# Kernel tuning notes

Hardware: AMD Instinct MI355X
Metric: run time of the kernel (lower is better)

Reference implementation:

```python
import jax, jax.numpy as jnp
import numpy as np

B, D_IN, D_Z, D_H, D_T, D_REC = 8192, 1024, 256, 256, 16, 256


def _softplus_beta(x, beta):
    # torch F.softplus(x, beta) = (1/beta) * log(1 + exp(beta*x))
    return jax.nn.softplus(beta * x) / beta


def setup_inputs() -> dict:
    key = jax.random.key(0)
    ks = jax.random.split(key, 17)
    w = lambda k, o, i: jax.random.normal(k, (o, i), jnp.float32) * (1.0 / np.sqrt(i))
    return {
        "I_t": jax.random.uniform(ks[0], (B, D_IN), jnp.float32),
        "h_m_1": jax.random.uniform(ks[1], (B, D_H), jnp.float32),
        "z_m_1": jax.random.uniform(ks[2], (B, D_Z), jnp.float32),
        "theta_m_1": jax.random.normal(ks[3], (B, D_T), jnp.float32),
        "eps_z": jax.random.normal(ks[4], (B, D_Z), jnp.float32),
        "eps_zhat": jax.random.normal(ks[5], (B, D_Z), jnp.float32),
        "W_post_mu": w(ks[6], D_Z, D_IN),
        "W_post_lv": w(ks[7], D_Z, D_IN),
        "W_z2h": w(ks[8], D_H, D_Z),
        "W_h2h": w(ks[9], D_H, D_H),
        "W_prior_mu": w(ks[10], D_Z, D_H),
        "W_prior_lv": w(ks[11], D_Z, D_H),
        "W_i2t": w(ks[12], D_T, D_IN),
        "W_vip2t": w(ks[13], D_T, D_Z),
        "W_t2z": w(ks[14], D_Z, D_T),
        "W_rec1": w(ks[15], D_REC, D_Z),
        "W_rec2": w(ks[16], D_IN, D_REC),
    }


def reference(I_t, h_m_1, z_m_1, theta_m_1, eps_z, eps_zhat,
              W_post_mu, W_post_lv, W_z2h, W_h2h, W_prior_mu, W_prior_lv,
              W_i2t, W_vip2t, W_t2z, W_rec1, W_rec2):
    relu = jax.nn.relu
    # prior pathway (perception_only=True branch)
    mu_p = relu(h_m_1 @ W_prior_mu.T)                       # [B, D_Z]
    sigma_p = _softplus_beta(h_m_1 @ W_prior_lv.T, 1.2)     # [B, D_Z]
    # theta dynamics; vip_to_theta has Positive parametrization -> relu(W)
    theta_h = (0.5 * theta_m_1 + 0.1 * (I_t @ W_i2t.T)
               - jax.lax.stop_gradient(sigma_p) @ relu(W_vip2t).T)  # [B, D_T]
    theta = 0.001 * _softplus_beta(theta_h, 0.5)
    # posterior + reparameterized sample
    mu_q = relu(I_t @ W_post_mu.T)
    sigma_q = relu(I_t @ W_post_lv.T)
    raw_z = jnp.clip(mu_q + eps_z * sigma_q, 0.0, 1.0)
    thresholds = 10.0 * (theta @ relu(W_t2z).T)             # Positive parametrization
    z = relu(raw_z - thresholds)                            # [B, D_Z]
    # reconstruction (two bias-free linears + sigmoid)
    I_hat = jax.nn.sigmoid((z @ W_rec1.T) @ W_rec2.T)       # [B, D_IN]
    # higher-state update and prior sample
    h = relu(z_m_1 @ W_z2h.T + h_m_1 @ W_h2h.T)             # [B, D_H]
    z_hat = mu_p + eps_zhat * sigma_p                       # [B, D_Z]
    # losses (as in torch forward)
    spatial = jnp.mean((I_t - I_hat) ** 2)
    temporal = jnp.mean((jax.lax.stop_gradient(z) - z_hat) ** 2)
    energy = jnp.mean(jnp.abs(z))
    return (I_hat, z, h, z_hat, spatial, temporal, energy)
```

## Files before the change

kernel.cpp:

```cpp
#include <hip/hip_runtime.h>
#include <math.h>

#define BB 8192
#define DIN 1024
#define DZ 256
#define DH 256
#define DT 16
#define DREC 256

#define OFF_IHAT 0
#define OFF_Z    (BB * DIN)
#define OFF_H    (OFF_Z + BB * DZ)
#define OFF_ZHAT (OFF_H + BB * DH)
#define OFF_SCAL (OFF_ZHAT + BB * DZ)

typedef unsigned short u16;
typedef __attribute__((ext_vector_type(8))) unsigned short u16x8;
typedef __attribute__((ext_vector_type(8))) __bf16 bf16x8;
typedef __attribute__((ext_vector_type(4))) float f32x4;

#define WS_HBF   0
#define WS_ZM1BF 2097152
#define WS_W     4194304
#define W_PM  (WS_W + 0)
#define W_PL  (W_PM + 262144)
#define W_Z2H (W_PL + 262144)
#define W_H2H (W_Z2H + 65536)
#define W_PRM (W_H2H + 65536)
#define W_PRL (W_PRM + 65536)
#define W_I2T (W_PRL + 65536)
#define W_VIP (W_I2T + 16384)
#define W_R1  (W_VIP + 4096)
#define W_R2  (W_R1 + 65536)
#define WS_THETA_BYTES 10657792

#define LDA 72

__device__ inline u16 f2bf(float f) {
  unsigned u = __builtin_bit_cast(unsigned, f);
  u += 0x7fff + ((u >> 16) & 1);
  return (u16)(u >> 16);
}

__device__ inline float softplus_stable(float y) {
  return (y > 20.f) ? y : log1pf(expf(y));
}

__device__ inline float block_sum256(float v, float* rbuf) {
#pragma unroll
  for (int off = 32; off > 0; off >>= 1) v += __shfl_down(v, off, 64);
  __syncthreads();
  if ((threadIdx.x & 63) == 0) rbuf[threadIdx.x >> 6] = v;
  __syncthreads();
  return rbuf[0] + rbuf[1] + rbuf[2] + rbuf[3];
}

__global__ __launch_bounds__(256) void k_cvt(
    const float* __restrict__ I_t, const float* __restrict__ h_m_1,
    const float* __restrict__ z_m_1, const float* __restrict__ Wpm,
    const float* __restrict__ Wpl, const float* __restrict__ Wz2h,
    const float* __restrict__ Wh2h, const float* __restrict__ Wprm,
    const float* __restrict__ Wprl, const float* __restrict__ Wi2t,
    const float* __restrict__ Wv, const float* __restrict__ Wr1,
    const float* __restrict__ Wr2, u16* __restrict__ dstI,
    u16* __restrict__ dstW) {
  const int S1 = 8388608, S2 = 10485760, S3 = 12582912, S4 = 12845056,
            S5 = 13107200, S6 = 13172736, S7 = 13238272, S8 = 13303808,
            S9 = 13369344, S10 = 13385728, S11 = 13389824, S12 = 13455360,
            S13 = 13717504;
  int nchunk = S13 / 8;
  for (int c = blockIdx.x * 256 + threadIdx.x; c < nchunk;
       c += gridDim.x * 256) {
    int f = c * 8;
    const float* src;
    float scale = 1.f;
    bool nrelu = false;
    u16* dst;
    if (f < S1)       { src = I_t  + f;        dst = dstI + f; }
    else {
      dst = dstW + (f - S1);
      if (f < S2)       src = h_m_1 + (f - S1);
      else if (f < S3)  src = z_m_1 + (f - S2);
      else if (f < S4)  src = Wpm  + (f - S3);
      else if (f < S5)  src = Wpl  + (f - S4);
      else if (f < S6)  src = Wz2h + (f - S5);
      else if (f < S7)  src = Wh2h + (f - S6);
      else if (f < S8)  src = Wprm + (f - S7);
      else if (f < S9)  src = Wprl + (f - S8);
      else if (f < S10) { src = Wi2t + (f - S9);  scale = 0.1f; }
      else if (f < S11) { src = Wv   + (f - S10); nrelu = true; }
      else if (f < S12) src = Wr1  + (f - S11);
      else              src = Wr2  + (f - S12);
    }
    float4 v0 = *(const float4*)(src);
    float4 v1 = *(const float4*)(src + 4);
    float vals[8] = {v0.x, v0.y, v0.z, v0.w, v1.x, v1.y, v1.z, v1.w};
    u16x8 o;
#pragma unroll
    for (int j = 0; j < 8; ++j) {
      float x = vals[j];
      x = nrelu ? -fmaxf(x, 0.f) : x * scale;
      o[j] = f2bf(x);
    }
    *(u16x8*)(dst) = o;
  }
}

template <int K, bool TWO>
__device__ inline void mfma_gemm(const u16* __restrict__ A,
                                 const u16* __restrict__ B0,
                                 const u16* __restrict__ B1, int row0,
                                 int col0, f32x4 (&acc)[2][4],
                                 f32x4 (&acc2)[2][4], u16* As, u16* Bs0,
                                 u16* Bs1) {
  const int tid = threadIdx.x;
  const int lane = tid & 63;
  const int w = tid >> 6;
  const int frow = lane & 15;
  const int fq = lane >> 4;

  for (int k0 = 0; k0 < K; k0 += 64) {
    __syncthreads();
#pragma unroll
    for (int i = 0; i < 4; ++i) {
      int c = tid + 256 * i;
      int r = c >> 3, kc = c & 7;
      u16x8 v = *(const u16x8*)(A + (size_t)(row0 + r) * K + k0 + kc * 8);
      *(u16x8*)(As + r * LDA + kc * 8) = v;
    }
#pragma unroll
    for (int i = 0; i < 2; ++i) {
      int c = tid + 256 * i;
      int r = c >> 3, kc = c & 7;
      *(u16x8*)(Bs0 + r * LDA + kc * 8) =
          *(const u16x8*)(B0 + (size_t)(col0 + r) * K + k0 + kc * 8);
      if (TWO)
        *(u16x8*)(Bs1 + r * LDA + kc * 8) =
            *(const u16x8*)(B1 + (size_t)(col0 + r) * K + k0 + kc * 8);
    }
    __syncthreads();
#pragma unroll
    for (int ks = 0; ks < 2; ++ks) {
      bf16x8 af[2], bf[4], bf2[4];
#pragma unroll
      for (int mi = 0; mi < 2; ++mi)
        af[mi] = __builtin_bit_cast(
            bf16x8, *(const u16x8*)(As + (w * 32 + mi * 16 + frow) * LDA +
                                    fq * 8 + ks * 32));
#pragma unroll
      for (int ni = 0; ni < 4; ++ni) {
        bf[ni] = __builtin_bit_cast(
            bf16x8,
            *(const u16x8*)(Bs0 + (ni * 16 + frow) * LDA + fq * 8 + ks * 32));
        if (TWO)
          bf2[ni] = __builtin_bit_cast(
              bf16x8, *(const u16x8*)(Bs1 + (ni * 16 + frow) * LDA + fq * 8 +
                                      ks * 32));
      }
#pragma unroll
      for (int mi = 0; mi < 2; ++mi)
#pragma unroll
        for (int ni = 0; ni < 4; ++ni) {
          acc[mi][ni] = __builtin_amdgcn_mfma_f32_16x16x32_bf16(
              af[mi], bf[ni], acc[mi][ni], 0, 0, 0);
          if (TWO)
            acc2[mi][ni] = __builtin_amdgcn_mfma_f32_16x16x32_bf16(
                af[mi], bf2[ni], acc2[mi][ni], 0, 0, 0);
        }
    }
  }
}

#define EPILOGUE_IDX()                          \
  const int tid = threadIdx.x;                  \
  const int lane = tid & 63;                    \
  const int w = tid >> 6;                       \
  const int frow = lane & 15;                   \
  const int fq = lane >> 4;                     \
  (void)tid

__global__ __launch_bounds__(256) void k_h(const u16* __restrict__ zm1_bf,
                                           const u16* __restrict__ h_bf,
                                           const u16* __restrict__ Wz2h,
                                           const u16* __restrict__ Wh2h,
                                           float* __restrict__ h_out) {
  __shared__ __align__(16) u16 As[128 * LDA];
  __shared__ __align__(16) u16 Bs0[64 * LDA];
  int col0 = blockIdx.x * 64, row0 = blockIdx.y * 128;
  f32x4 acc[2][4];
#pragma unroll
  for (int mi = 0; mi < 2; ++mi)
#pragma unroll
    for (int ni = 0; ni < 4; ++ni) acc[mi][ni] = (f32x4){0.f, 0.f, 0.f, 0.f};
  mfma_gemm<DZ, false>(zm1_bf, Wz2h, nullptr, row0, col0, acc, acc, As, Bs0, Bs0);
  mfma_gemm<DH, false>(h_bf, Wh2h, nullptr, row0, col0, acc, acc, As, Bs0, Bs0);
  EPILOGUE_IDX();
#pragma unroll
  for (int mi = 0; mi < 2; ++mi)
#pragma unroll
    for (int ni = 0; ni < 4; ++ni)
#pragma unroll
      for (int r = 0; r < 4; ++r) {
        int m = row0 + w * 32 + mi * 16 + fq * 4 + r;
        int n = col0 + ni * 16 + frow;
        h_out[(size_t)m * DH + n] = fmaxf(acc[mi][ni][r], 0.f);
      }
}

__global__ __launch_bounds__(256) void k_prior(
    const u16* __restrict__ h_bf, const u16* __restrict__ Wpm,
    const u16* __restrict__ Wpl, const float* __restrict__ eps_zhat,
    float* __restrict__ zhat_out, u16* __restrict__ sigma_bf) {
  __shared__ __align__(16) u16 As[128 * LDA];
  __shared__ __align__(16) u16 Bs0[64 * LDA];
  __shared__ __align__(16) u16 Bs1[64 * LDA];
  int col0 = blockIdx.x * 64, row0 = blockIdx.y * 128;
  f32x4 acc[2][4], acc2[2][4];
#pragma unroll
  for (int mi = 0; mi < 2; ++mi)
#pragma unroll
    for (int ni = 0; ni < 4; ++ni) {
      acc[mi][ni] = (f32x4){0.f, 0.f, 0.f, 0.f};
      acc2[mi][ni] = (f32x4){0.f, 0.f, 0.f, 0.f};
    }
  mfma_gemm<DH, true>(h_bf, Wpm, Wpl, row0, col0, acc, acc2, As, Bs0, Bs1);
  EPILOGUE_IDX();
#pragma unroll
  for (int mi = 0; mi < 2; ++mi)
#pragma unroll
    for (int ni = 0; ni < 4; ++ni)
#pragma unroll
      for (int r = 0; r < 4; ++r) {
        int m = row0 + w * 32 + mi * 16 + fq * 4 + r;
        int n = col0 + ni * 16 + frow;
        float mu = fmaxf(acc[mi][ni][r], 0.f);
        float sig = softplus_stable(1.2f * acc2[mi][ni][r]) * (1.f / 1.2f);
        zhat_out[(size_t)m * DZ + n] =
            mu + eps_zhat[(size_t)m * DZ + n] * sig;
        sigma_bf[(size_t)m * DZ + n] = f2bf(sig);
      }
}

__global__ __launch_bounds__(256) void k_theta(
    const u16* __restrict__ I_bf, const u16* __restrict__ Wi2t,
    const u16* __restrict__ sigma_bf, const u16* __restrict__ Wv,
    const float* __restrict__ theta_m_1, float* __restrict__ theta_ws) {
  const int tid = threadIdx.x;
  const int lane = tid & 63;
  const int w = tid >> 6;
  const int frow = lane & 15;
  const int fq = lane >> 4;
  const int m0 = blockIdx.x * 64 + w * 16;
  f32x4 acc = (f32x4){0.f, 0.f, 0.f, 0.f};
  const u16* arow = I_bf + (size_t)(m0 + frow) * DIN + fq * 8;
  const u16* brow = Wi2t + (size_t)frow * DIN + fq * 8;
#pragma unroll
  for (int ks = 0; ks < DIN / 32; ++ks) {
    bf16x8 a = __builtin_bit_cast(bf16x8, *(const u16x8*)(arow + ks * 32));
    bf16x8 b = __builtin_bit_cast(bf16x8, *(const u16x8*)(brow + ks * 32));
    acc = __builtin_amdgcn_mfma_f32_16x16x32_bf16(a, b, acc, 0, 0, 0);
  }
  const u16* arow2 = sigma_bf + (size_t)(m0 + frow) * DZ + fq * 8;
  const u16* brow2 = Wv + (size_t)frow * DZ + fq * 8;
#pragma unroll
  for (int ks = 0; ks < DZ / 32; ++ks) {
    bf16x8 a = __builtin_bit_cast(bf16x8, *(const u16x8*)(arow2 + ks * 32));
    bf16x8 b = __builtin_bit_cast(bf16x8, *(const u16x8*)(brow2 + ks * 32));
    acc = __builtin_amdgcn_mfma_f32_16x16x32_bf16(a, b, acc, 0, 0, 0);
  }
#pragma unroll
  for (int r = 0; r < 4; ++r) {
    int m = m0 + fq * 4 + r;
    float th = 0.5f * theta_m_1[(size_t)m * DT + frow] + acc[r];
    theta_ws[(size_t)m * DT + frow] = 0.002f * softplus_stable(0.5f * th);
  }
}

__global__ __launch_bounds__(256) void k_post(
    const u16* __restrict__ I_bf, const u16* __restrict__ Wpm,
    const u16* __restrict__ Wpl, const float* __restrict__ eps_z,
    const float* __restrict__ theta_ws, const float* __restrict__ W_t2z,
    const float* __restrict__ zhat, float* __restrict__ z_out,
    u16* __restrict__ z_bf, float* __restrict__ scal) {
  __shared__ __align__(16) u16 As[128 * LDA];
  __shared__ __align__(16) u16 Bs0[64 * LDA];
  __shared__ __align__(16) u16 Bs1[64 * LDA];
  __shared__ float rbuf[4];
  int col0 = blockIdx.x * 64, row0 = blockIdx.y * 128;
  f32x4 acc[2][4], acc2[2][4];
#pragma unroll
  for (int mi = 0; mi < 2; ++mi)
#pragma unroll
    for (int ni = 0; ni < 4; ++ni) {
      acc[mi][ni] = (f32x4){0.f, 0.f, 0.f, 0.f};
      acc2[mi][ni] = (f32x4){0.f, 0.f, 0.f, 0.f};
    }
  mfma_gemm<DIN, true>(I_bf, Wpm, Wpl, row0, col0, acc, acc2, As, Bs0, Bs1);
  EPILOGUE_IDX();
  __syncthreads();
  float* th_s = (float*)As;
  float* wt_s = (float*)Bs0;
  for (int idx = tid; idx < 128 * 16; idx += 256) {
    int r = idx >> 4, j = idx & 15;
    th_s[r * 17 + j] = theta_ws[(size_t)(row0 + r) * DT + j];
  }
  for (int idx = tid; idx < 64 * 16; idx += 256) {
    int n = idx >> 4, j = idx & 15;
    wt_s[n * 17 + j] = 10.f * fmaxf(W_t2z[(col0 + n) * DT + j], 0.f);
  }
  __syncthreads();
  float tsum = 0.f, esum = 0.f;
#pragma unroll
  for (int mi = 0; mi < 2; ++mi)
#pragma unroll
    for (int ni = 0; ni < 4; ++ni)
#pragma unroll
      for (int r = 0; r < 4; ++r) {
        int lr = w * 32 + mi * 16 + fq * 4 + r;
        int ln = ni * 16 + frow;
        int m = row0 + lr;
        int n = col0 + ln;
        float mu = fmaxf(acc[mi][ni][r], 0.f);
        float sq = fmaxf(acc2[mi][ni][r], 0.f);
        float raw = mu + eps_z[(size_t)m * DZ + n] * sq;
        raw = fminf(fmaxf(raw, 0.f), 1.f);
        float thr = 0.f;
#pragma unroll
        for (int j = 0; j < 16; ++j)
          thr = fmaf(th_s[lr * 17 + j], wt_s[ln * 17 + j], thr);
        float zz = fmaxf(raw - thr, 0.f);
        z_out[(size_t)m * DZ + n] = zz;
        z_bf[(size_t)m * DZ + n] = f2bf(zz);
        float d = zz - zhat[(size_t)m * DZ + n];
        tsum += d * d;
        esum += zz;
      }
  float t = block_sum256(tsum, rbuf);
  if (tid == 0) atomicAdd(scal + 1, t * (1.f / ((float)BB * DZ)));
  float e = block_sum256(esum, rbuf);
  if (tid == 0) atomicAdd(scal + 2, e * (1.f / ((float)BB * DZ)));
}

__global__ __launch_bounds__(256) void k_rec1(const u16* __restrict__ z_bf,
                                              const u16* __restrict__ Wr1,
                                              u16* __restrict__ r1_bf) {
  __shared__ __align__(16) u16 As[128 * LDA];
  __shared__ __align__(16) u16 Bs0[64 * LDA];
  int col0 = blockIdx.x * 64, row0 = blockIdx.y * 128;
  f32x4 acc[2][4];
#pragma unroll
  for (int mi = 0; mi < 2; ++mi)
#pragma unroll
    for (int ni = 0; ni < 4; ++ni) acc[mi][ni] = (f32x4){0.f, 0.f, 0.f, 0.f};
  mfma_gemm<DZ, false>(z_bf, Wr1, nullptr, row0, col0, acc, acc, As, Bs0, Bs0);
  EPILOGUE_IDX();
#pragma unroll
  for (int mi = 0; mi < 2; ++mi)
#pragma unroll
    for (int ni = 0; ni < 4; ++ni)
#pragma unroll
      for (int r = 0; r < 4; ++r) {
        int m = row0 + w * 32 + mi * 16 + fq * 4 + r;
        int n = col0 + ni * 16 + frow;
        r1_bf[(size_t)m * DREC + n] = f2bf(acc[mi][ni][r]);
      }
}

__global__ __launch_bounds__(256) void k_rec2(const u16* __restrict__ r1_bf,
                                              const u16* __restrict__ Wr2,
                                              const float* __restrict__ I_t,
                                              float* __restrict__ ihat_out,
                                              float* __restrict__ scal) {
  __shared__ __align__(16) u16 As[128 * LDA];
  __shared__ __align__(16) u16 Bs0[64 * LDA];
  __shared__ float rbuf[4];
  int col0 = blockIdx.x * 64, row0 = blockIdx.y * 128;
  f32x4 acc[2][4];
#pragma unroll
  for (int mi = 0; mi < 2; ++mi)
#pragma unroll
    for (int ni = 0; ni < 4; ++ni) acc[mi][ni] = (f32x4){0.f, 0.f, 0.f, 0.f};
  mfma_gemm<DREC, false>(r1_bf, Wr2, nullptr, row0, col0, acc, acc, As, Bs0, Bs0);
  EPILOGUE_IDX();
  float lsum = 0.f;
#pragma unroll
  for (int mi = 0; mi < 2; ++mi)
#pragma unroll
    for (int ni = 0; ni < 4; ++ni)
#pragma unroll
      for (int r = 0; r < 4; ++r) {
        int m = row0 + w * 32 + mi * 16 + fq * 4 + r;
        int n = col0 + ni * 16 + frow;
        float ih = 1.f / (1.f + expf(-acc[mi][ni][r]));
        ihat_out[(size_t)m * DIN + n] = ih;
        float d = I_t[(size_t)m * DIN + n] - ih;
        lsum += d * d;
      }
  float s = block_sum256(lsum, rbuf);
  if (tid == 0) atomicAdd(scal + 0, s * (1.f / ((float)BB * DIN)));
}

extern "C" void kernel_launch(void* const* d_in, const int* in_sizes, int n_in,
                              void* d_out, int out_size, void* d_ws,
                              size_t ws_size, hipStream_t stream) {
  const float* I_t       = (const float*)d_in[0];
  const float* h_m_1     = (const float*)d_in[1];
  const float* z_m_1     = (const float*)d_in[2];
  const float* theta_m_1 = (const float*)d_in[3];
  const float* eps_z     = (const float*)d_in[4];
  const float* eps_zhat  = (const float*)d_in[5];
  const float* W_post_mu = (const float*)d_in[6];
  const float* W_post_lv = (const float*)d_in[7];
  const float* W_z2h     = (const float*)d_in[8];
  const float* W_h2h     = (const float*)d_in[9];
  const float* W_prior_mu= (const float*)d_in[10];
  const float* W_prior_lv= (const float*)d_in[11];
  const float* W_i2t     = (const float*)d_in[12];
  const float* W_vip2t   = (const float*)d_in[13];
  const float* W_t2z     = (const float*)d_in[14];
  const float* W_rec1    = (const float*)d_in[15];
  const float* W_rec2    = (const float*)d_in[16];

  float* out = (float*)d_out;
  float* ihat = out + OFF_IHAT;
  float* zout = out + OFF_Z;
  float* hout = out + OFF_H;
  float* zhat = out + OFF_ZHAT;
  float* scal = out + OFF_SCAL;

  u16* ws_u = (u16*)d_ws;
  u16* I_bf = (u16*)ihat;
  u16* h_bf = ws_u + WS_HBF;
  u16* zm1_bf = ws_u + WS_ZM1BF;
  u16* sigma_bf = zm1_bf;
  u16* r1_bf = zm1_bf;
  u16* z_bf = h_bf;
  float* theta_ws = (float*)((char*)d_ws + WS_THETA_BYTES);

  hipMemsetAsync(scal, 0, 3 * sizeof(float), stream);

  k_cvt<<<2048, 256, 0, stream>>>(I_t, h_m_1, z_m_1, W_post_mu, W_post_lv,
                                  W_z2h, W_h2h, W_prior_mu, W_prior_lv, W_i2t,
                                  W_vip2t, W_rec1, W_rec2, I_bf,
                                  ws_u + WS_HBF);

  dim3 g256(DZ / 64, BB / 128);
  dim3 g1024(DIN / 64, BB / 128);

  k_h<<<g256, 256, 0, stream>>>(zm1_bf, h_bf, ws_u + W_Z2H, ws_u + W_H2H, hout);
  k_prior<<<g256, 256, 0, stream>>>(h_bf, ws_u + W_PRM, ws_u + W_PRL, eps_zhat,
                                    zhat, sigma_bf);
  k_theta<<<BB / 64, 256, 0, stream>>>(I_bf, ws_u + W_I2T, sigma_bf,
                                       ws_u + W_VIP, theta_m_1, theta_ws);
  k_post<<<g256, 256, 0, stream>>>(I_bf, ws_u + W_PM, ws_u + W_PL, eps_z,
                                   theta_ws, W_t2z, zhat, zout, z_bf, scal);
  k_rec1<<<g256, 256, 0, stream>>>(z_bf, ws_u + W_R1, r1_bf);
  k_rec2<<<g1024, 256, 0, stream>>>(r1_bf, ws_u + W_R2, I_t, ihat, scal);
}
```

Measured before the change: 285.1 us.

## Fuse fp32-to-bf16 conversion into GEMM staging and merge kernels

Removes the separate conversion kernel and instead converts fp32 inputs and weights to bf16 while staging tiles into LDS inside each GEMM. The h, prior and theta computations are fused: k_hp computes h and the prior from a shared h_m_1 tile, and k_post computes theta in-kernel alongside the posterior GEMM, cutting the launch count from seven to four. Tiles shrink from 128 to 64 rows, which doubles the grid size. The cost is that I_t and the weights are now read as fp32 and reconverted by every block that uses them, and each staged fp32 load is wider.

```diff
diff --git a/kernel.cpp b/kernel.cpp
--- a/kernel.cpp
+++ b/kernel.cpp
@@ -14,27 +14,16 @@
 #define OFF_ZHAT (OFF_H + BB * DH)
 #define OFF_SCAL (OFF_ZHAT + BB * DZ)
 
+#define WS_SIGMA 0
+#define WS_ZBF   2097152
+#define WS_R1    4194304
+
+#define LDA 72
+
 typedef unsigned short u16;
 typedef __attribute__((ext_vector_type(8))) unsigned short u16x8;
 typedef __attribute__((ext_vector_type(8))) __bf16 bf16x8;
 typedef __attribute__((ext_vector_type(4))) float f32x4;
-
-#define WS_HBF   0
-#define WS_ZM1BF 2097152
-#define WS_W     4194304
-#define W_PM  (WS_W + 0)
-#define W_PL  (W_PM + 262144)
-#define W_Z2H (W_PL + 262144)
-#define W_H2H (W_Z2H + 65536)
-#define W_PRM (W_H2H + 65536)
-#define W_PRL (W_PRM + 65536)
-#define W_I2T (W_PRL + 65536)
-#define W_VIP (W_I2T + 16384)
-#define W_R1  (W_VIP + 4096)
-#define W_R2  (W_R1 + 65536)
-#define WS_THETA_BYTES 10657792
-
-#define LDA 72
 
 __device__ inline u16 f2bf(float f) {
   unsigned u = __builtin_bit_cast(unsigned, f);
@@ -55,45 +44,44 @@
   return rbuf[0] + rbuf[1] + rbuf[2] + rbuf[3];
 }
 
-__global__ __launch_bounds__(256) void k_cvt(
-    const float* __restrict__ I_t, const float* __restrict__ h_m_1,
-    const float* __restrict__ z_m_1, const float* __restrict__ Wpm,
-    const float* __restrict__ Wpl, const float* __restrict__ Wz2h,
-    const float* __restrict__ Wh2h, const float* __restrict__ Wprm,
-    const float* __restrict__ Wprl, const float* __restrict__ Wi2t,
-    const float* __restrict__ Wv, const float* __restrict__ Wr1,
-    const float* __restrict__ Wr2, u16* __restrict__ dstI,
-    u16* __restrict__ dstW) {
-  const int S1 = 8388608, S2 = 10485760, S3 = 12582912, S4 = 12845056,
-            S5 = 13107200, S6 = 13172736, S7 = 13238272, S8 = 13303808,
-            S9 = 13369344, S10 = 13385728, S11 = 13389824, S12 = 13455360,
-            S13 = 13717504;
-  int nchunk = S13 / 8;
-  for (int c = blockIdx.x * 256 + threadIdx.x; c < nchunk;
-       c += gridDim.x * 256) {
-    int f = c * 8;
-    const float* src;
-    float scale = 1.f;
-    bool nrelu = false;
-    u16* dst;
-    if (f < S1)       { src = I_t  + f;        dst = dstI + f; }
-    else {
-      dst = dstW + (f - S1);
-      if (f < S2)       src = h_m_1 + (f - S1);
-      else if (f < S3)  src = z_m_1 + (f - S2);
-      else if (f < S4)  src = Wpm  + (f - S3);
-      else if (f < S5)  src = Wpl  + (f - S4);
-      else if (f < S6)  src = Wz2h + (f - S5);
-      else if (f < S7)  src = Wh2h + (f - S6);
-      else if (f < S8)  src = Wprm + (f - S7);
-      else if (f < S9)  src = Wprl + (f - S8);
-      else if (f < S10) { src = Wi2t + (f - S9);  scale = 0.1f; }
-      else if (f < S11) { src = Wv   + (f - S10); nrelu = true; }
-      else if (f < S12) src = Wr1  + (f - S11);
-      else              src = Wr2  + (f - S12);
-    }
-    float4 v0 = *(const float4*)(src);
-    float4 v1 = *(const float4*)(src + 4);
+__device__ inline void stage64(u16* lds, const float* __restrict__ src,
+                               int row0, int ld, int k0, float scale) {
+  const int tid = threadIdx.x;
+#pragma unroll
+  for (int i = 0; i < 2; ++i) {
+    int idx = tid + 256 * i;
+    int r = idx >> 3, kc = idx & 7;
+    const float* p = src + (size_t)(row0 + r) * ld + k0 + kc * 8;
+    float4 v0 = *(const float4*)p;
+    float4 v1 = *(const float4*)(p + 4);
+    float vals[8] = {v0.x, v0.y, v0.z, v0.w, v1.x, v1.y, v1.z, v1.w};
+    u16x8 o;
+#pragma unroll
+    for (int j = 0; j < 8; ++j) o[j] = f2bf(vals[j] * scale);
+    *(u16x8*)(lds + r * LDA + kc * 8) = o;
+  }
+}
+
+__device__ inline void stage64_bf(u16* lds, const u16* __restrict__ src,
+                                  int row0, int ld, int k0) {
+  const int tid = threadIdx.x;
+#pragma unroll
+  for (int i = 0; i < 2; ++i) {
+    int idx = tid + 256 * i;
+    int r = idx >> 3, kc = idx & 7;
+    *(u16x8*)(lds + r * LDA + kc * 8) =
+        *(const u16x8*)(src + (size_t)(row0 + r) * ld + k0 + kc * 8);
+  }
+}
+
+__device__ inline void stage16(u16* lds, const float* __restrict__ src, int ld,
+                               int k0, float scale, bool nrelu) {
+  const int tid = threadIdx.x;
+  if (tid < 128) {
+    int r = tid >> 3, kc = tid & 7;
+    const float* p = src + (size_t)r * ld + k0 + kc * 8;
+    float4 v0 = *(const float4*)p;
+    float4 v1 = *(const float4*)(p + 4);
     float vals[8] = {v0.x, v0.y, v0.z, v0.w, v1.x, v1.y, v1.z, v1.w};
     u16x8 o;
 #pragma unroll
@@ -102,207 +90,141 @@
       x = nrelu ? -fmaxf(x, 0.f) : x * scale;
       o[j] = f2bf(x);
     }
-    *(u16x8*)(dst) = o;
-  }
-}
-
-template <int K, bool TWO>
-__device__ inline void mfma_gemm(const u16* __restrict__ A,
-                                 const u16* __restrict__ B0,
-                                 const u16* __restrict__ B1, int row0,
-                                 int col0, f32x4 (&acc)[2][4],
-                                 f32x4 (&acc2)[2][4], u16* As, u16* Bs0,
-                                 u16* Bs1) {
-  const int tid = threadIdx.x;
-  const int lane = tid & 63;
-  const int w = tid >> 6;
-  const int frow = lane & 15;
-  const int fq = lane >> 4;
-
-  for (int k0 = 0; k0 < K; k0 += 64) {
-    __syncthreads();
-#pragma unroll
-    for (int i = 0; i < 4; ++i) {
-      int c = tid + 256 * i;
-      int r = c >> 3, kc = c & 7;
-      u16x8 v = *(const u16x8*)(A + (size_t)(row0 + r) * K + k0 + kc * 8);
-      *(u16x8*)(As + r * LDA + kc * 8) = v;
-    }
-#pragma unroll
-    for (int i = 0; i < 2; ++i) {
-      int c = tid + 256 * i;
-      int r = c >> 3, kc = c & 7;
-      *(u16x8*)(Bs0 + r * LDA + kc * 8) =
-          *(const u16x8*)(B0 + (size_t)(col0 + r) * K + k0 + kc * 8);
-      if (TWO)
-        *(u16x8*)(Bs1 + r * LDA + kc * 8) =
-            *(const u16x8*)(B1 + (size_t)(col0 + r) * K + k0 + kc * 8);
-    }
-    __syncthreads();
-#pragma unroll
-    for (int ks = 0; ks < 2; ++ks) {
-      bf16x8 af[2], bf[4], bf2[4];
-#pragma unroll
-      for (int mi = 0; mi < 2; ++mi)
-        af[mi] = __builtin_bit_cast(
-            bf16x8, *(const u16x8*)(As + (w * 32 + mi * 16 + frow) * LDA +
-                                    fq * 8 + ks * 32));
+    *(u16x8*)(lds + r * LDA + kc * 8) = o;
+  }
+}
+
+__device__ inline bf16x8 frag(const u16* lds, int row, int off) {
+  return __builtin_bit_cast(bf16x8, *(const u16x8*)(lds + row * LDA + off));
+}
+
+#define MFMA __builtin_amdgcn_mfma_f32_16x16x32_bf16
+
+__global__ __launch_bounds__(256) void k_hp(
+    const float* __restrict__ h_m_1, const float* __restrict__ z_m_1,
+    const float* __restrict__ Wh2h, const float* __restrict__ Wprm,
+    const float* __restrict__ Wprl, const float* __restrict__ Wz2h,
+    const float* __restrict__ eps_zhat, float* __restrict__ h_out,
+    float* __restrict__ zhat_out, u16* __restrict__ sigma_bf) {
+  __shared__ __align__(16) u16 As[64 * LDA], B0s[64 * LDA], B1s[64 * LDA],
+      B2s[64 * LDA];
+  const int col0 = blockIdx.x * 64, row0 = blockIdx.y * 64;
+  const int tid = threadIdx.x, lane = tid & 63, w = tid >> 6;
+  const int frow = lane & 15, fq = lane >> 4;
+  f32x4 acch[4], accm[4], accs[4];
+#pragma unroll
+  for (int ni = 0; ni < 4; ++ni) {
+    acch[ni] = (f32x4){0.f, 0.f, 0.f, 0.f};
+    accm[ni] = (f32x4){0.f, 0.f, 0.f, 0.f};
+    accs[ni] = (f32x4){0.f, 0.f, 0.f, 0.f};
+  }
+  for (int k0 = 0; k0 < DH; k0 += 64) {
+    __syncthreads();
+    stage64(As, h_m_1, row0, DH, k0, 1.f);
+    stage64(B0s, Wh2h, col0, DH, k0, 1.f);
+    stage64(B1s, Wprm, col0, DH, k0, 1.f);
+    stage64(B2s, Wprl, col0, DH, k0, 1.f);
+    __syncthreads();
+#pragma unroll
+    for (int ks = 0; ks < 2; ++ks) {
+      int off = ks * 32 + fq * 8;
+      bf16x8 a = frag(As, w * 16 + frow, off);
 #pragma unroll
       for (int ni = 0; ni < 4; ++ni) {
-        bf[ni] = __builtin_bit_cast(
-            bf16x8,
-            *(const u16x8*)(Bs0 + (ni * 16 + frow) * LDA + fq * 8 + ks * 32));
-        if (TWO)
-          bf2[ni] = __builtin_bit_cast(
-              bf16x8, *(const u16x8*)(Bs1 + (ni * 16 + frow) * LDA + fq * 8 +
-                                      ks * 32));
+        acch[ni] = MFMA(a, frag(B0s, ni * 16 + frow, off), acch[ni], 0, 0, 0);
+        accm[ni] = MFMA(a, frag(B1s, ni * 16 + frow, off), accm[ni], 0, 0, 0);
+        accs[ni] = MFMA(a, frag(B2s, ni * 16 + frow, off), accs[ni], 0, 0, 0);
       }
-#pragma unroll
-      for (int mi = 0; mi < 2; ++mi)
-#pragma unroll
-        for (int ni = 0; ni < 4; ++ni) {
-          acc[mi][ni] = __builtin_amdgcn_mfma_f32_16x16x32_bf16(
-              af[mi], bf[ni], acc[mi][ni], 0, 0, 0);
-          if (TWO)
-            acc2[mi][ni] = __builtin_amdgcn_mfma_f32_16x16x32_bf16(
-                af[mi], bf2[ni], acc2[mi][ni], 0, 0, 0);
-        }
-    }
-  }
-}
-
-#define EPILOGUE_IDX()                          \
-  const int tid = threadIdx.x;                  \
-  const int lane = tid & 63;                    \
-  const int w = tid >> 6;                       \
-  const int frow = lane & 15;                   \
-  const int fq = lane >> 4;                     \
-  (void)tid
-
-__global__ __launch_bounds__(256) void k_h(const u16* __restrict__ zm1_bf,
-                                           const u16* __restrict__ h_bf,
-                                           const u16* __restrict__ Wz2h,
-                                           const u16* __restrict__ Wh2h,
-                                           float* __restrict__ h_out) {
-  __shared__ __align__(16) u16 As[128 * LDA];
-  __shared__ __align__(16) u16 Bs0[64 * LDA];
-  int col0 = blockIdx.x * 64, row0 = blockIdx.y * 128;
-  f32x4 acc[2][4];
-#pragma unroll
-  for (int mi = 0; mi < 2; ++mi)
-#pragma unroll
-    for (int ni = 0; ni < 4; ++ni) acc[mi][ni] = (f32x4){0.f, 0.f, 0.f, 0.f};
-  mfma_gemm<DZ, false>(zm1_bf, Wz2h, nullptr, row0, col0, acc, acc, As, Bs0, Bs0);
-  mfma_gemm<DH, false>(h_bf, Wh2h, nullptr, row0, col0, acc, acc, As, Bs0, Bs0);
-  EPILOGUE_IDX();
-#pragma unroll
-  for (int mi = 0; mi < 2; ++mi)
-#pragma unroll
-    for (int ni = 0; ni < 4; ++ni)
-#pragma unroll
-      for (int r = 0; r < 4; ++r) {
-        int m = row0 + w * 32 + mi * 16 + fq * 4 + r;
-        int n = col0 + ni * 16 + frow;
-        h_out[(size_t)m * DH + n] = fmaxf(acc[mi][ni][r], 0.f);
+    }
+  }
+  for (int k0 = 0; k0 < DZ; k0 += 64) {
+    __syncthreads();
+    stage64(As, z_m_1, row0, DZ, k0, 1.f);
+    stage64(B0s, Wz2h, col0, DZ, k0, 1.f);
+    __syncthreads();
+#pragma unroll
+    for (int ks = 0; ks < 2; ++ks) {
+      int off = ks * 32 + fq * 8;
+      bf16x8 a = frag(As, w * 16 + frow, off);
+#pragma unroll
+      for (int ni = 0; ni < 4; ++ni)
+        acch[ni] = MFMA(a, frag(B0s, ni * 16 + frow, off), acch[ni], 0, 0, 0);
+    }
+  }
+#pragma unroll
+  for (int ni = 0; ni < 4; ++ni)
+#pragma unroll
+    for (int r = 0; r < 4; ++r) {
+      int m = row0 + w * 16 + fq * 4 + r;
+      int n = col0 + ni * 16 + frow;
+      h_out[(size_t)m * DH + n] = fmaxf(acch[ni][r], 0.f);
+      float sig = softplus_stable(1.2f * accs[ni][r]) * (1.f / 1.2f);
+      float mu = fmaxf(accm[ni][r], 0.f);
+      zhat_out[(size_t)m * DZ + n] = mu + eps_zhat[(size_t)m * DZ + n] * sig;
+      sigma_bf[(size_t)m * DZ + n] = f2bf(sig);
+    }
+}
+
+__global__ __launch_bounds__(256) void k_post(
+    const float* __restrict__ I_t, const float* __restrict__ Wpm,
+    const float* __restrict__ Wpl, const float* __restrict__ Wi2t,
+    const float* __restrict__ Wv, const u16* __restrict__ sigma_bf,
+    const float* __restrict__ theta_m_1, const float* __restrict__ W_t2z,
+    const float* __restrict__ eps_z, const float* __restrict__ zhat,
+    float* __restrict__ z_out, u16* __restrict__ z_bf,
+    float* __restrict__ scal) {
+  __shared__ __align__(16) u16 As[64 * LDA], B0s[64 * LDA], B1s[64 * LDA],
+      Bts[16 * LDA];
+  __shared__ float rbuf[4];
+  const int col0 = blockIdx.x * 64, row0 = blockIdx.y * 64;
+  const int tid = threadIdx.x, lane = tid & 63, w = tid >> 6;
+  const int frow = lane & 15, fq = lane >> 4;
+  f32x4 accm[4], accs[4];
+  f32x4 acct = (f32x4){0.f, 0.f, 0.f, 0.f};
+#pragma unroll
+  for (int ni = 0; ni < 4; ++ni) {
+    accm[ni] = (f32x4){0.f, 0.f, 0.f, 0.f};
+    accs[ni] = (f32x4){0.f, 0.f, 0.f, 0.f};
+  }
+  for (int k0 = 0; k0 < DIN; k0 += 64) {
+    __syncthreads();
+    stage64(As, I_t, row0, DIN, k0, 1.f);
+    stage64(B0s, Wpm, col0, DIN, k0, 1.f);
+    stage64(B1s, Wpl, col0, DIN, k0, 1.f);
+    stage16(Bts, Wi2t, DIN, k0, 0.1f, false);
+    __syncthreads();
+#pragma unroll
+    for (int ks = 0; ks < 2; ++ks) {
+      int off = ks * 32 + fq * 8;
+      bf16x8 a = frag(As, w * 16 + frow, off);
+#pragma unroll
+      for (int ni = 0; ni < 4; ++ni) {
+        accm[ni] = MFMA(a, frag(B0s, ni * 16 + frow, off), accm[ni], 0, 0, 0);
+        accs[ni] = MFMA(a, frag(B1s, ni * 16 + frow, off), accs[ni], 0, 0, 0);
       }
-}
-
-__global__ __launch_bounds__(256) void k_prior(
-    const u16* __restrict__ h_bf, const u16* __restrict__ Wpm,
-    const u16* __restrict__ Wpl, const float* __restrict__ eps_zhat,
-    float* __restrict__ zhat_out, u16* __restrict__ sigma_bf) {
-  __shared__ __align__(16) u16 As[128 * LDA];
-  __shared__ __align__(16) u16 Bs0[64 * LDA];
-  __shared__ __align__(16) u16 Bs1[64 * LDA];
-  int col0 = blockIdx.x * 64, row0 = blockIdx.y * 128;
-  f32x4 acc[2][4], acc2[2][4];
-#pragma unroll
-  for (int mi = 0; mi < 2; ++mi)
-#pragma unroll
-    for (int ni = 0; ni < 4; ++ni) {
-      acc[mi][ni] = (f32x4){0.f, 0.f, 0.f, 0.f};
-      acc2[mi][ni] = (f32x4){0.f, 0.f, 0.f, 0.f};
-    }
-  mfma_gemm<DH, true>(h_bf, Wpm, Wpl, row0, col0, acc, acc2, As, Bs0, Bs1);
-  EPILOGUE_IDX();
-#pragma unroll
-  for (int mi = 0; mi < 2; ++mi)
-#pragma unroll
-    for (int ni = 0; ni < 4; ++ni)
-#pragma unroll
-      for (int r = 0; r < 4; ++r) {
-        int m = row0 + w * 32 + mi * 16 + fq * 4 + r;
-        int n = col0 + ni * 16 + frow;
-        float mu = fmaxf(acc[mi][ni][r], 0.f);
-        float sig = softplus_stable(1.2f * acc2[mi][ni][r]) * (1.f / 1.2f);
-        zhat_out[(size_t)m * DZ + n] =
-            mu + eps_zhat[(size_t)m * DZ + n] * sig;
-        sigma_bf[(size_t)m * DZ + n] = f2bf(sig);
-      }
-}
-
-__global__ __launch_bounds__(256) void k_theta(
-    const u16* __restrict__ I_bf, const u16* __restrict__ Wi2t,
-    const u16* __restrict__ sigma_bf, const u16* __restrict__ Wv,
-    const float* __restrict__ theta_m_1, float* __restrict__ theta_ws) {
-  const int tid = threadIdx.x;
-  const int lane = tid & 63;
-  const int w = tid >> 6;
-  const int frow = lane & 15;
-  const int fq = lane >> 4;
-  const int m0 = blockIdx.x * 64 + w * 16;
-  f32x4 acc = (f32x4){0.f, 0.f, 0.f, 0.f};
-  const u16* arow = I_bf + (size_t)(m0 + frow) * DIN + fq * 8;
-  const u16* brow = Wi2t + (size_t)frow * DIN + fq * 8;
-#pragma unroll
-  for (int ks = 0; ks < DIN / 32; ++ks) {
-    bf16x8 a = __builtin_bit_cast(bf16x8, *(const u16x8*)(arow + ks * 32));
-    bf16x8 b = __builtin_bit_cast(bf16x8, *(const u16x8*)(brow + ks * 32));
-    acc = __builtin_amdgcn_mfma_f32_16x16x32_bf16(a, b, acc, 0, 0, 0);
-  }
-  const u16* arow2 = sigma_bf + (size_t)(m0 + frow) * DZ + fq * 8;
-  const u16* brow2 = Wv + (size_t)frow * DZ + fq * 8;
-#pragma unroll
-  for (int ks = 0; ks < DZ / 32; ++ks) {
-    bf16x8 a = __builtin_bit_cast(bf16x8, *(const u16x8*)(arow2 + ks * 32));
-    bf16x8 b = __builtin_bit_cast(bf16x8, *(const u16x8*)(brow2 + ks * 32));
-    acc = __builtin_amdgcn_mfma_f32_16x16x32_bf16(a, b, acc, 0, 0, 0);
-  }
-#pragma unroll
-  for (int r = 0; r < 4; ++r) {
-    int m = m0 + fq * 4 + r;
-    float th = 0.5f * theta_m_1[(size_t)m * DT + frow] + acc[r];
-    theta_ws[(size_t)m * DT + frow] = 0.002f * softplus_stable(0.5f * th);
-  }
-}
-
-__global__ __launch_bounds__(256) void k_post(
-    const u16* __restrict__ I_bf, const u16* __restrict__ Wpm,
-    const u16* __restrict__ Wpl, const float* __restrict__ eps_z,
-    const float* __restrict__ theta_ws, const float* __restrict__ W_t2z,
-    const float* __restrict__ zhat, float* __restrict__ z_out,
-    u16* __restrict__ z_bf, float* __restrict__ scal) {
-  __shared__ __align__(16) u16 As[128 * LDA];
-  __shared__ __align__(16) u16 Bs0[64 * LDA];
-  __shared__ __align__(16) u16 Bs1[64 * LDA];
-  __shared__ float rbuf[4];
-  int col0 = blockIdx.x * 64, row0 = blockIdx.y * 128;
-  f32x4 acc[2][4], acc2[2][4];
-#pragma unroll
-  for (int mi = 0; mi < 2; ++mi)
-#pragma unroll
-    for (int ni = 0; ni < 4; ++ni) {
-      acc[mi][ni] = (f32x4){0.f, 0.f, 0.f, 0.f};
-      acc2[mi][ni] = (f32x4){0.f, 0.f, 0.f, 0.f};
-    }
-  mfma_gemm<DIN, true>(I_bf, Wpm, Wpl, row0, col0, acc, acc2, As, Bs0, Bs1);
-  EPILOGUE_IDX();
+      acct = MFMA(a, frag(Bts, frow, off), acct, 0, 0, 0);
+    }
+  }
+  for (int k0 = 0; k0 < DZ; k0 += 64) {
+    __syncthreads();
+    stage64_bf(As, sigma_bf, row0, DZ, k0);
+    stage16(Bts, Wv, DZ, k0, 1.f, true);
+    __syncthreads();
+#pragma unroll
+    for (int ks = 0; ks < 2; ++ks) {
+      int off = ks * 32 + fq * 8;
+      acct = MFMA(frag(As, w * 16 + frow, off), frag(Bts, frow, off), acct, 0,
+                  0, 0);
+    }
+  }
   __syncthreads();
   float* th_s = (float*)As;
-  float* wt_s = (float*)Bs0;
-  for (int idx = tid; idx < 128 * 16; idx += 256) {
-    int r = idx >> 4, j = idx & 15;
-    th_s[r * 17 + j] = theta_ws[(size_t)(row0 + r) * DT + j];
+  float* wt_s = (float*)B0s;
+#pragma unroll
+  for (int r = 0; r < 4; ++r) {
+    int lr = w * 16 + fq * 4 + r;
+    float th = 0.5f * theta_m_1[(size_t)(row0 + lr) * DT + frow] + acct[r];
+    th_s[lr * 17 + frow] = 0.002f * softplus_stable(0.5f * th);
   }
   for (int idx = tid; idx < 64 * 16; idx += 256) {
     int n = idx >> 4, j = idx & 15;
@@ -311,30 +233,28 @@
   __syncthreads();
   float tsum = 0.f, esum = 0.f;
 #pragma unroll
-  for (int mi = 0; mi < 2; ++mi)
-#pragma unroll
-    for (int ni = 0; ni < 4; ++ni)
-#pragma unroll
-      for (int r = 0; r < 4; ++r) {
-        int lr = w * 32 + mi * 16 + fq * 4 + r;
-        int ln = ni * 16 + frow;
-        int m = row0 + lr;
-        int n = col0 + ln;
-        float mu = fmaxf(acc[mi][ni][r], 0.f);
-        float sq = fmaxf(acc2[mi][ni][r], 0.f);
-        float raw = mu + eps_z[(size_t)m * DZ + n] * sq;
-        raw = fminf(fmaxf(raw, 0.f), 1.f);
-        float thr = 0.f;
-#pragma unroll
-        for (int j = 0; j < 16; ++j)
-          thr = fmaf(th_s[lr * 17 + j], wt_s[ln * 17 + j], thr);
-        float zz = fmaxf(raw - thr, 0.f);
-        z_out[(size_t)m * DZ + n] = zz;
-        z_bf[(size_t)m * DZ + n] = f2bf(zz);
-        float d = zz - zhat[(size_t)m * DZ + n];
-        tsum += d * d;
-        esum += zz;
-      }
+  for (int ni = 0; ni < 4; ++ni)
+#pragma unroll
+    for (int r = 0; r < 4; ++r) {
+      int lr = w * 16 + fq * 4 + r;
+      int ln = ni * 16 + frow;
+      int m = row0 + lr;
+      int n = col0 + ln;
+      float mu = fmaxf(accm[ni][r], 0.f);
+      float sq = fmaxf(accs[ni][r], 0.f);
+      float raw = mu + eps_z[(size_t)m * DZ + n] * sq;
+      raw = fminf(fmaxf(raw, 0.f), 1.f);
+      float thr = 0.f;
+#pragma unroll
+      for (int j = 0; j < 16; ++j)
+        thr = fmaf(th_s[lr * 17 + j], wt_s[ln * 17 + j], thr);
+      float zz = fmaxf(raw - thr, 0.f);
+      z_out[(size_t)m * DZ + n] = zz;
+      z_bf[(size_t)m * DZ + n] = f2bf(zz);
+      float d = zz - zhat[(size_t)m * DZ + n];
+      tsum += d * d;
+      esum += zz;
+    }
   float t = block_sum256(tsum, rbuf);
   if (tid == 0) atomicAdd(scal + 1, t * (1.f / ((float)BB * DZ)));
   float e = block_sum256(esum, rbuf);
@@ -342,60 +262,78 @@
 }
 
 __global__ __launch_bounds__(256) void k_rec1(const u16* __restrict__ z_bf,
-                                              const u16* __restrict__ Wr1,
+                                              const float* __restrict__ Wr1,
                                               u16* __restrict__ r1_bf) {
-  __shared__ __align__(16) u16 As[128 * LDA];
-  __shared__ __align__(16) u16 Bs0[64 * LDA];
-  int col0 = blockIdx.x * 64, row0 = blockIdx.y * 128;
-  f32x4 acc[2][4];
-#pragma unroll
-  for (int mi = 0; mi < 2; ++mi)
-#pragma unroll
-    for (int ni = 0; ni < 4; ++ni) acc[mi][ni] = (f32x4){0.f, 0.f, 0.f, 0.f};
-  mfma_gemm<DZ, false>(z_bf, Wr1, nullptr, row0, col0, acc, acc, As, Bs0, Bs0);
-  EPILOGUE_IDX();
-#pragma unroll
-  for (int mi = 0; mi < 2; ++mi)
-#pragma unroll
-    for (int ni = 0; ni < 4; ++ni)
-#pragma unroll
-      for (int r = 0; r < 4; ++r) {
-        int m = row0 + w * 32 + mi * 16 + fq * 4 + r;
-        int n = col0 + ni * 16 + frow;
-        r1_bf[(size_t)m * DREC + n] = f2bf(acc[mi][ni][r]);
-      }
+  __shared__ __align__(16) u16 As[64 * LDA], B0s[64 * LDA];
+  const int col0 = blockIdx.x * 64, row0 = blockIdx.y * 64;
+  const int tid = threadIdx.x, lane = tid & 63, w = tid >> 6;
+  const int frow = lane & 15, fq = lane >> 4;
+  f32x4 acc[4];
+#pragma unroll
+  for (int ni = 0; ni < 4; ++ni) acc[ni] = (f32x4){0.f, 0.f, 0.f, 0.f};
+  for (int k0 = 0; k0 < DZ; k0 += 64) {
+    __syncthreads();
+    stage64_bf(As, z_bf, row0, DZ, k0);
+    stage64(B0s, Wr1, col0, DZ, k0, 1.f);
+    __syncthreads();
+#pragma unroll
+    for (int ks = 0; ks < 2; ++ks) {
+      int off = ks * 32 + fq * 8;
+      bf16x8 a = frag(As, w * 16 + frow, off);
+#pragma unroll
+      for (int ni = 0; ni < 4; ++ni)
+        acc[ni] = MFMA(a, frag(B0s, ni * 16 + frow, off), acc[ni], 0, 0, 0);
+    }
+  }
+#pragma unroll
+  for (int ni = 0; ni < 4; ++ni)
+#pragma unroll
+    for (int r = 0; r < 4; ++r) {
+      int m = row0 + w * 16 + fq * 4 + r;
+      int n = col0 + ni * 16 + frow;
+      r1_bf[(size_t)m * DREC + n] = f2bf(acc[ni][r]);
+    }
 }
 
 __global__ __launch_bounds__(256) void k_rec2(const u16* __restrict__ r1_bf,
-                                              const u16* __restrict__ Wr2,
+                                              const float* __restrict__ Wr2,
                                               const float* __restrict__ I_t,
                                               float* __restrict__ ihat_out,
                                               float* __restrict__ scal) {
-  __shared__ __align__(16) u16 As[128 * LDA];
-  __shared__ __align__(16) u16 Bs0[64 * LDA];
+  __shared__ __align__(16) u16 As[64 * LDA], B0s[64 * LDA];
   __shared__ float rbuf[4];
-  int col0 = blockIdx.x * 64, row0 = blockIdx.y * 128;
-  f32x4 acc[2][4];
-#pragma unroll
-  for (int mi = 0; mi < 2; ++mi)
-#pragma unroll
-    for (int ni = 0; ni < 4; ++ni) acc[mi][ni] = (f32x4){0.f, 0.f, 0.f, 0.f};
-  mfma_gemm<DREC, false>(r1_bf, Wr2, nullptr, row0, col0, acc, acc, As, Bs0, Bs0);
-  EPILOGUE_IDX();
+  const int col0 = blockIdx.x * 64, row0 = blockIdx.y * 64;
+  const int tid = threadIdx.x, lane = tid & 63, w = tid >> 6;
+  const int frow = lane & 15, fq = lane >> 4;
+  f32x4 acc[4];
+#pragma unroll
+  for (int ni = 0; ni < 4; ++ni) acc[ni] = (f32x4){0.f, 0.f, 0.f, 0.f};
+  for (int k0 = 0; k0 < DREC; k0 += 64) {
+    __syncthreads();
+    stage64_bf(As, r1_bf, row0, DREC, k0);
+    stage64(B0s, Wr2, col0, DREC, k0, 1.f);
+    __syncthreads();
+#pragma unroll
+    for (int ks = 0; ks < 2; ++ks) {
+      int off = ks * 32 + fq * 8;
+      bf16x8 a = frag(As, w * 16 + frow, off);
+#pragma unroll
+      for (int ni = 0; ni < 4; ++ni)
+        acc[ni] = MFMA(a, frag(B0s, ni * 16 + frow, off), acc[ni], 0, 0, 0);
+    }
+  }
   float lsum = 0.f;
 #pragma unroll
-  for (int mi = 0; mi < 2; ++mi)
-#pragma unroll
-    for (int ni = 0; ni < 4; ++ni)
-#pragma unroll
-      for (int r = 0; r < 4; ++r) {
-        int m = row0 + w * 32 + mi * 16 + fq * 4 + r;
-        int n = col0 + ni * 16 + frow;
-        float ih = 1.f / (1.f + expf(-acc[mi][ni][r]));
-        ihat_out[(size_t)m * DIN + n] = ih;
-        float d = I_t[(size_t)m * DIN + n] - ih;
-        lsum += d * d;
-      }
+  for (int ni = 0; ni < 4; ++ni)
+#pragma unroll
+    for (int r = 0; r < 4; ++r) {
+      int m = row0 + w * 16 + fq * 4 + r;
+      int n = col0 + ni * 16 + frow;
+      float ih = 1.f / (1.f + expf(-acc[ni][r]));
+      ihat_out[(size_t)m * DIN + n] = ih;
+      float d = I_t[(size_t)m * DIN + n] - ih;
+      lsum += d * d;
+    }
   float s = block_sum256(lsum, rbuf);
   if (tid == 0) atomicAdd(scal + 0, s * (1.f / ((float)BB * DIN)));
 }
@@ -429,31 +367,20 @@
   float* scal = out + OFF_SCAL;
 
   u16* ws_u = (u16*)d_ws;
-  u16* I_bf = (u16*)ihat;
-  u16* h_bf = ws_u + WS_HBF;
-  u16* zm1_bf = ws_u + WS_ZM1BF;
-  u16* sigma_bf = zm1_bf;
-  u16* r1_bf = zm1_bf;
-  u16* z_bf = h_bf;
-  float* theta_ws = (float*)((char*)d_ws + WS_THETA_BYTES);
+  u16* sigma_bf = ws_u + WS_SIGMA;
+  u16* z_bf = ws_u + WS_ZBF;
+  u16* r1_bf = ws_u + WS_R1;
 
   hipMemsetAsync(scal, 0, 3 * sizeof(float), stream);
 
-  k_cvt<<<2048, 256, 0, stream>>>(I_t, h_m_1, z_m_1, W_post_mu, W_post_lv,
-                                  W_z2h, W_h2h, W_prior_mu, W_prior_lv, W_i2t,
-                                  W_vip2t, W_rec1, W_rec2, I_bf,
-                                  ws_u + WS_HBF);
-
-  dim3 g256(DZ / 64, BB / 128);
-  dim3 g1024(DIN / 64, BB / 128);
-
-  k_h<<<g256, 256, 0, stream>>>(zm1_bf, h_bf, ws_u + W_Z2H, ws_u + W_H2H, hout);
-  k_prior<<<g256, 256, 0, stream>>>(h_bf, ws_u + W_PRM, ws_u + W_PRL, eps_zhat,
-                                    zhat, sigma_bf);
-  k_theta<<<BB / 64, 256, 0, stream>>>(I_bf, ws_u + W_I2T, sigma_bf,
-                                       ws_u + W_VIP, theta_m_1, theta_ws);
-  k_post<<<g256, 256, 0, stream>>>(I_bf, ws_u + W_PM, ws_u + W_PL, eps_z,
-                                   theta_ws, W_t2z, zhat, zout, z_bf, scal);
-  k_rec1<<<g256, 256, 0, stream>>>(z_bf, ws_u + W_R1, r1_bf);
-  k_rec2<<<g1024, 256, 0, stream>>>(r1_bf, ws_u + W_R2, I_t, ihat, scal);
-}
+  dim3 gz(DZ / 64, BB / 64);
+  dim3 gi(DIN / 64, BB / 64);
+
+  k_hp<<<gz, 256, 0, stream>>>(h_m_1, z_m_1, W_h2h, W_prior_mu, W_prior_lv,
+                               W_z2h, eps_zhat, hout, zhat, sigma_bf);
+  k_post<<<gz, 256, 0, stream>>>(I_t, W_post_mu, W_post_lv, W_i2t, W_vip2t,
+                                 sigma_bf, theta_m_1, W_t2z, eps_z, zhat, zout,
+                                 z_bf, scal);
+  k_rec1<<<gz, 256, 0, stream>>>(z_bf, W_rec1, r1_bf);
+  k_rec2<<<gi, 256, 0, stream>>>(r1_bf, W_rec2, I_t, ihat, scal);
+}
```

New measurement: 322.6 us. +13.1%, slower.
